# Kernel optimization log

Hardware: AMD Instinct MI355X
Metric: run time of the kernel (lower is better)

Reference implementation:

```python
import jax, jax.numpy as jnp
import numpy as np

TAU = 0.5  # routing_temperature


def setup_inputs() -> dict:
    key = jax.random.key(0)
    ks = jax.random.split(key, 12)
    B, N, D = 8, 4096, 384  # d_inner = 384, grid 64x64
    G = 4
    s = 0.02
    inp = {
        "x": jax.random.normal(ks[0], (B, N, D), dtype=jnp.float32),
        "W_stream1": jax.random.normal(ks[1], (D, D), dtype=jnp.float32) * s,
        "b_stream1": jnp.zeros((D,), dtype=jnp.float32),
        "W_stream2": jax.random.normal(ks[2], (D, G), dtype=jnp.float32) * s,
        "b_stream2": jnp.zeros((G,), dtype=jnp.float32),
        "self_bias": jnp.full((1, G, 1, 1), 2.0, dtype=jnp.float32),
        "W_ga": jax.random.normal(ks[3], (D, D), dtype=jnp.float32) * s,
        "b_ga": jnp.full((D,), 1.5, dtype=jnp.float32),
        "W_gb": jax.random.normal(ks[4], (D, D), dtype=jnp.float32) * s,
        "b_gb": jnp.full((D,), -1.5, dtype=jnp.float32),
        "W_inj": jax.random.normal(ks[5], (D, 2 * D), dtype=jnp.float32) * s,
        "W_state": jax.random.normal(ks[6], (D, 2 * D), dtype=jnp.float32) * s,
        "W_out": jax.random.normal(ks[7], (2 * D, D), dtype=jnp.float32) * s,
        "D_skip": jnp.ones((D,), dtype=jnp.float32),
        "k_steps": 4,
    }
    return inp


def reference(x, W_stream1, b_stream1, W_stream2, b_stream2, self_bias,
              W_ga, b_ga, W_gb, b_gb, W_inj, W_state, W_out, D_skip, k_steps):
    B, N, D = x.shape
    h = w = int(round(N ** 0.5))
    G = self_bias.shape[1]
    C = D // G

    def to_grid(t):  # (B, N, F) -> (B, F, h, w)
        return jnp.transpose(t, (0, 2, 1)).reshape(B, -1, h, w)

    # state (U, V)
    uv = x @ W_state
    u, v = jnp.split(uv, 2, axis=-1)
    u, v = to_grid(u), to_grid(v)

    # stream function -> divergence-free velocity (discrete curl)
    psi = to_grid(jax.nn.silu(x @ W_stream1 + b_stream1) @ W_stream2 + b_stream2)
    psi_h = jnp.pad(psi, ((0, 0), (0, 0), (1, 1), (0, 0)))
    vx = 0.5 * (psi_h[:, :, 2:, :] - psi_h[:, :, :-2, :])
    psi_w = jnp.pad(psi, ((0, 0), (0, 0), (0, 0), (1, 1)))
    vy = -0.5 * (psi_w[:, :, :, 2:] - psi_w[:, :, :, :-2])

    # 5-neighbor routing: [self, up, down, left, right]
    logits = jnp.stack([
        jnp.broadcast_to(self_bias, vx.shape),
        -vx / TAU, vx / TAU, -vy / TAU, vy / TAU,
    ], axis=2)  # (B, G, 5, h, w)
    routing = jax.nn.softmax(logits, axis=2)

    gate_a = to_grid(jax.nn.sigmoid(x @ W_ga + b_ga))
    gate_b = to_grid(jax.nn.sigmoid(x @ W_gb + b_gb))

    inj = x @ W_inj
    xu, xv = jnp.split(inj, 2, axis=-1)
    xu, xv = to_grid(xu), to_grid(xv)

    def transport(state):  # (B, D, h, w)
        sp_h = jnp.pad(state, ((0, 0), (0, 0), (1, 1), (0, 0)))
        s_up, s_down = sp_h[:, :, :-2, :], sp_h[:, :, 2:, :]
        sp_w = jnp.pad(state, ((0, 0), (0, 0), (0, 0), (1, 1)))
        s_left, s_right = sp_w[:, :, :, :-2], sp_w[:, :, :, 2:]
        nb = jnp.stack([state, s_up, s_down, s_left, s_right], axis=2)  # (B,D,5,h,w)
        nb = nb.reshape(B, G, C, 5, h, w)
        out = jnp.einsum('bgcnhw,bgnhw->bgchw', nb, routing)
        return out.reshape(B, D, h, w)

    for _ in range(int(k_steps)):
        u = gate_a * transport(u) + gate_b * xu
        v = gate_a * transport(v) + gate_b * xv

    u_out = jnp.transpose(u.reshape(B, D, N), (0, 2, 1))
    v_out = jnp.transpose(v.reshape(B, D, N), (0, 2, 1))
    combined = jnp.concatenate([u_out, v_out], axis=-1)
    return combined @ W_out + x * D_skip
```

## Files before the change

### kernel.cpp

```cpp
#include <hip/hip_runtime.h>
#include <hip/hip_bf16.h>

typedef __attribute__((ext_vector_type(8))) short bf16x8;
typedef __attribute__((ext_vector_type(4))) short short4v;
typedef __attribute__((ext_vector_type(4))) float f32x4;

#define TAU_INV 2.0f

__device__ __forceinline__ short f2bf(float f) {
  unsigned u = __float_as_uint(f);
  u += 0x7fffu + ((u >> 16) & 1u);
  return (short)(u >> 16);
}
__device__ __forceinline__ float bf2f(short s) {
  return __uint_as_float(((unsigned)(unsigned short)s) << 16);
}

__global__ __launch_bounds__(256) void prep_weights(
    const float* __restrict__ w_state, const float* __restrict__ w_inj,
    const float* __restrict__ w_ga, const float* __restrict__ w_gb,
    const float* __restrict__ w_s1, const float* __restrict__ w_out,
    short* __restrict__ t_state, short* __restrict__ t_inj,
    short* __restrict__ t_ga, short* __restrict__ t_gb,
    short* __restrict__ t_s1, short* __restrict__ t_out)
{
  int idx = blockIdx.x * 256 + threadIdx.x;
  const float* src; short* dst; int C, K;
  if (idx < 294912)                  { src = w_state; dst = t_state; C = 768; K = 384; }
  else if ((idx -= 294912) < 294912) { src = w_inj;   dst = t_inj;   C = 768; K = 384; }
  else if ((idx -= 294912) < 147456) { src = w_ga;    dst = t_ga;    C = 384; K = 384; }
  else if ((idx -= 147456) < 147456) { src = w_gb;    dst = t_gb;    C = 384; K = 384; }
  else if ((idx -= 147456) < 147456) { src = w_s1;    dst = t_s1;    C = 384; K = 384; }
  else           { idx -= 147456;      src = w_out;   dst = t_out;   C = 384; K = 768; }
  int c = idx / K, k = idx - c * K;
  dst[c * K + k] = f2bf(src[k * C + c]);
}

template<int EP>
__global__ __launch_bounds__(256) void gemm_x(
    const float* __restrict__ X, const short* __restrict__ Wt,
    const float* __restrict__ bias,
    short* __restrict__ out0, short* __restrict__ out1)
{
  __shared__ short As[128 * 72];
  __shared__ short Bs[128 * 72];
  const int tid = threadIdx.x;
  const int lane = tid & 63;
  const int wv = tid >> 6;
  const int wr = wv >> 1, wc = wv & 1;
  const int m0 = blockIdx.x * 128, c0 = blockIdx.y * 128;
  const int l15 = lane & 15, l4 = lane >> 4;
  f32x4 acc[4][4] = {};
  for (int k0 = 0; k0 < 384; k0 += 64) {
    __syncthreads();
#pragma unroll
    for (int i = 0; i < 8; ++i) {
      int q = tid + i * 256;
      int m = q >> 4, kq = (q & 15) * 4;
      const float4 xv = *(const float4*)(X + (m0 + m) * 384 + k0 + kq);
      short4v s;
      s[0] = f2bf(xv.x); s[1] = f2bf(xv.y); s[2] = f2bf(xv.z); s[3] = f2bf(xv.w);
      *(short4v*)(As + m * 72 + kq) = s;
    }
#pragma unroll
    for (int i = 0; i < 4; ++i) {
      int h = tid + i * 256;
      int c = h >> 3, kc = (h & 7) * 8;
      bf16x8 wvv = *(const bf16x8*)(Wt + (c0 + c) * 384 + k0 + kc);
      *(bf16x8*)(Bs + c * 72 + kc) = wvv;
    }
    __syncthreads();
#pragma unroll
    for (int kk = 0; kk < 2; ++kk) {
      bf16x8 af[4], bfv[4];
#pragma unroll
      for (int f = 0; f < 4; ++f) {
        af[f]  = *(const bf16x8*)(As + (wr * 64 + f * 16 + l15) * 72 + kk * 32 + l4 * 8);
        bfv[f] = *(const bf16x8*)(Bs + (wc * 64 + f * 16 + l15) * 72 + kk * 32 + l4 * 8);
      }
#pragma unroll
      for (int i = 0; i < 4; ++i)
#pragma unroll
        for (int j = 0; j < 4; ++j)
          acc[i][j] = __builtin_amdgcn_mfma_f32_16x16x32_bf16(af[i], bfv[j], acc[i][j], 0, 0, 0);
    }
  }
#pragma unroll
  for (int i = 0; i < 4; ++i) {
#pragma unroll
    for (int j = 0; j < 4; ++j) {
      const int c = c0 + wc * 64 + j * 16 + l15;
      const int mb = m0 + wr * 64 + i * 16 + l4 * 4;
      f32x4 v = acc[i][j];
      if (EP == 0) {
        short4v s;
        s[0] = f2bf(v[0]); s[1] = f2bf(v[1]); s[2] = f2bf(v[2]); s[3] = f2bf(v[3]);
        int b = mb >> 12, n = mb & 4095;
        short* base = (c < 384) ? out0 : out1;
        int plane = (c >= 384) ? (c - 384) : c;
        *(short4v*)(base + (b * 384 + plane) * 4096 + n) = s;
      } else if (EP == 1) {
        float bb = bias[c];
        short4v s;
#pragma unroll
        for (int r = 0; r < 4; ++r) {
          float t = v[r] + bb;
          t = 1.f / (1.f + __expf(-t));
          s[r] = f2bf(t);
        }
        int b = mb >> 12, n = mb & 4095;
        *(short4v*)(out0 + (b * 384 + c) * 4096 + n) = s;
      } else {
        float bb = bias[c];
#pragma unroll
        for (int r = 0; r < 4; ++r) {
          float t = v[r] + bb;
          float sg = 1.f / (1.f + __expf(-t));
          out0[(mb + r) * 384 + c] = f2bf(t * sg);
        }
      }
    }
  }
}

__global__ __launch_bounds__(256) void psi_kernel(
    const short* __restrict__ S1, const float* __restrict__ W2,
    const float* __restrict__ b2, float* __restrict__ psi)
{
  const int lane = threadIdx.x & 63;
  const int wv = threadIdx.x >> 6;
  const int m = blockIdx.x * 4 + wv;
  float a0 = 0.f, a1 = 0.f, a2 = 0.f, a3 = 0.f;
#pragma unroll
  for (int t = 0; t < 6; ++t) {
    int k = lane + t * 64;
    float sv = bf2f(S1[m * 384 + k]);
    float4 wr = *(const float4*)(W2 + k * 4);
    a0 += sv * wr.x; a1 += sv * wr.y; a2 += sv * wr.z; a3 += sv * wr.w;
  }
  for (int off = 32; off > 0; off >>= 1) {
    a0 += __shfl_down(a0, off, 64);
    a1 += __shfl_down(a1, off, 64);
    a2 += __shfl_down(a2, off, 64);
    a3 += __shfl_down(a3, off, 64);
  }
  if (lane == 0) {
    int bb = m >> 12, n = m & 4095;
    psi[(bb * 4 + 0) * 4096 + n] = a0 + b2[0];
    psi[(bb * 4 + 1) * 4096 + n] = a1 + b2[1];
    psi[(bb * 4 + 2) * 4096 + n] = a2 + b2[2];
    psi[(bb * 4 + 3) * 4096 + n] = a3 + b2[3];
  }
}

__global__ __launch_bounds__(256) void routing_kernel(
    const float* __restrict__ psi, const float* __restrict__ sb,
    float* __restrict__ R)
{
  const int idx = blockIdx.x * 256 + threadIdx.x;
  const int n = idx & 4095, bg = idx >> 12;
  const int i = n >> 6, j = n & 63;
  const float* p = psi + bg * 4096;
  float up = (i > 0)  ? p[n - 64] : 0.f;
  float dn = (i < 63) ? p[n + 64] : 0.f;
  float lf = (j > 0)  ? p[n - 1]  : 0.f;
  float rt = (j < 63) ? p[n + 1]  : 0.f;
  float vx = 0.5f * (dn - up);
  float vy = -0.5f * (rt - lf);
  float l0 = sb[bg & 3];
  float l1 = -vx * TAU_INV, l2 = vx * TAU_INV, l3 = -vy * TAU_INV, l4v = vy * TAU_INV;
  float mx = fmaxf(fmaxf(fmaxf(l0, l1), fmaxf(l2, l3)), l4v);
  float e0 = __expf(l0 - mx), e1 = __expf(l1 - mx), e2 = __expf(l2 - mx);
  float e3 = __expf(l3 - mx), e4 = __expf(l4v - mx);
  float inv = 1.f / (e0 + e1 + e2 + e3 + e4);
  const int NP = 8 * 4 * 4096;
  R[0 * NP + idx] = e0 * inv;
  R[1 * NP + idx] = e1 * inv;
  R[2 * NP + idx] = e2 * inv;
  R[3 * NP + idx] = e3 * inv;
  R[4 * NP + idx] = e4 * inv;
}

__global__ __launch_bounds__(512, 2) void transport_kernel(
    short* __restrict__ Ug, short* __restrict__ Vg,
    const short* __restrict__ Ga, const short* __restrict__ Gb,
    const short* __restrict__ Xu, const short* __restrict__ Xv,
    const float* __restrict__ R, const int* __restrict__ ksp)
{
  __shared__ float su[4096];
  __shared__ float sv[4096];
  const int tid = threadIdx.x;
  const int bd = blockIdx.x;
  const int b = bd / 384;
  const int d = bd - b * 384;
  const int g = d / 96;
  const int pbase = bd * 4096;
  const int rbase = (b * 4 + g) * 4096;
  const int NP = 8 * 4 * 4096;
  const int p0 = tid * 8;
  const int i = tid >> 3;
  const int j0 = (tid & 7) * 8;
  const int s = i & 7;

  float ga[8], gb[8], xu[8], xv[8], r0[8], r1[8], r2[8], r3[8], r4[8];
  {
    bf16x8 t;
    t = *(const bf16x8*)(Ga + pbase + p0);
#pragma unroll
    for (int c = 0; c < 8; ++c) ga[c] = bf2f(t[c]);
    t = *(const bf16x8*)(Gb + pbase + p0);
#pragma unroll
    for (int c = 0; c < 8; ++c) gb[c] = bf2f(t[c]);
    t = *(const bf16x8*)(Xu + pbase + p0);
#pragma unroll
    for (int c = 0; c < 8; ++c) xu[c] = bf2f(t[c]);
    t = *(const bf16x8*)(Xv + pbase + p0);
#pragma unroll
    for (int c = 0; c < 8; ++c) xv[c] = bf2f(t[c]);
  }
#pragma unroll
  for (int q = 0; q < 2; ++q) {
    float4 f0 = *(const float4*)(R + 0 * NP + rbase + p0 + q * 4);
    float4 f1 = *(const float4*)(R + 1 * NP + rbase + p0 + q * 4);
    float4 f2 = *(const float4*)(R + 2 * NP + rbase + p0 + q * 4);
    float4 f3 = *(const float4*)(R + 3 * NP + rbase + p0 + q * 4);
    float4 f4 = *(const float4*)(R + 4 * NP + rbase + p0 + q * 4);
    r0[q*4+0]=f0.x; r0[q*4+1]=f0.y; r0[q*4+2]=f0.z; r0[q*4+3]=f0.w;
    r1[q*4+0]=f1.x; r1[q*4+1]=f1.y; r1[q*4+2]=f1.z; r1[q*4+3]=f1.w;
    r2[q*4+0]=f2.x; r2[q*4+1]=f2.y; r2[q*4+2]=f2.z; r2[q*4+3]=f2.w;
    r3[q*4+0]=f3.x; r3[q*4+1]=f3.y; r3[q*4+2]=f3.z; r3[q*4+3]=f3.w;
    r4[q*4+0]=f4.x; r4[q*4+1]=f4.y; r4[q*4+2]=f4.z; r4[q*4+3]=f4.w;
  }
  {
    bf16x8 tu = *(const bf16x8*)(Ug + pbase + p0);
    bf16x8 tv = *(const bf16x8*)(Vg + pbase + p0);
#pragma unroll
    for (int c = 0; c < 8; ++c) { su[p0 + (c ^ s)] = bf2f(tu[c]); sv[p0 + (c ^ s)] = bf2f(tv[c]); }
  }
  __syncthreads();
  const int ks = ksp[0];
  const bool hasUp = (i > 0), hasDn = (i < 63);
  const int sU = (i - 1) & 7, sD = (i + 1) & 7;
  for (int step = 0; step < ks; ++step) {
    float cu[8], cv[8], nu[8], nv[8];
#pragma unroll
    for (int c = 0; c < 8; ++c) { cu[c] = su[p0 + (c ^ s)]; cv[c] = sv[p0 + (c ^ s)]; }
    float luu = (j0 > 0)  ? su[(p0 - 1) ^ s] : 0.f;
    float luv = (j0 > 0)  ? sv[(p0 - 1) ^ s] : 0.f;
    float ruu = (j0 < 56) ? su[(p0 + 8) ^ s] : 0.f;
    float ruv = (j0 < 56) ? sv[(p0 + 8) ^ s] : 0.f;
#pragma unroll
    for (int c = 0; c < 8; ++c) {
      float upU = hasUp ? su[(p0 - 64) + (c ^ sU)] : 0.f;
      float upV = hasUp ? sv[(p0 - 64) + (c ^ sU)] : 0.f;
      float dnU = hasDn ? su[(p0 + 64) + (c ^ sD)] : 0.f;
      float dnV = hasDn ? sv[(p0 + 64) + (c ^ sD)] : 0.f;
      float lfU = (c > 0) ? cu[c - 1] : luu;
      float lfV = (c > 0) ? cv[c - 1] : luv;
      float rtU = (c < 7) ? cu[c + 1] : ruu;
      float rtV = (c < 7) ? cv[c + 1] : ruv;
      nu[c] = ga[c] * (r0[c]*cu[c] + r1[c]*upU + r2[c]*dnU + r3[c]*lfU + r4[c]*rtU) + gb[c]*xu[c];
      nv[c] = ga[c] * (r0[c]*cv[c] + r1[c]*upV + r2[c]*dnV + r3[c]*lfV + r4[c]*rtV) + gb[c]*xv[c];
    }
    __syncthreads();
#pragma unroll
    for (int c = 0; c < 8; ++c) { su[p0 + (c ^ s)] = nu[c]; sv[p0 + (c ^ s)] = nv[c]; }
    __syncthreads();
  }
  bf16x8 ou, ov;
#pragma unroll
  for (int c = 0; c < 8; ++c) { ou[c] = f2bf(su[p0 + (c ^ s)]); ov[c] = f2bf(sv[p0 + (c ^ s)]); }
  *(bf16x8*)(Ug + pbase + p0) = ou;
  *(bf16x8*)(Vg + pbase + p0) = ov;
}

__global__ __launch_bounds__(256) void gemm_final(
    const short* __restrict__ U, const short* __restrict__ V,
    const short* __restrict__ Wt, const float* __restrict__ X,
    const float* __restrict__ Dskip, float* __restrict__ out)
{
  __shared__ short As[64 * 128];
  __shared__ short Bs[128 * 72];
  const int tid = threadIdx.x;
  const int lane = tid & 63;
  const int wv = tid >> 6, wr = wv >> 1, wc = wv & 1;
  const int m0 = blockIdx.x * 128, c0 = blockIdx.y * 128;
  const int b = m0 >> 12, n0 = m0 & 4095;
  const int l15 = lane & 15, l4 = lane >> 4;
  f32x4 acc[4][4] = {};
  for (int k0 = 0; k0 < 768; k0 += 64) {
    const short* src = (k0 < 384) ? U : V;
    const int kp = (k0 >= 384) ? (k0 - 384) : k0;
    __syncthreads();
#pragma unroll
    for (int i = 0; i < 4; ++i) {
      int h = tid + i * 256;
      int k = h >> 4, cc = h & 15;
      bf16x8 tv = *(const bf16x8*)(src + (b * 384 + kp + k) * 4096 + n0 + cc * 8);
      int ccs = cc ^ (((k >> 3) & 3) << 1);
      *(bf16x8*)(As + k * 128 + ccs * 8) = tv;
    }
#pragma unroll
    for (int i = 0; i < 4; ++i) {
      int h = tid + i * 256;
      int c = h >> 3, kc = (h & 7) * 8;
      bf16x8 wvv = *(const bf16x8*)(Wt + (c0 + c) * 768 + k0 + kc);
      *(bf16x8*)(Bs + c * 72 + kc) = wvv;
    }
    __syncthreads();
#pragma unroll
    for (int kk = 0; kk < 2; ++kk) {
      bf16x8 af[4], bfv[4];
#pragma unroll
      for (int f = 0; f < 4; ++f) {
        const int mm = wr * 64 + f * 16 + l15;
        const int chunk = mm >> 3, wi = mm & 7;
        bf16x8 av;
#pragma unroll
        for (int jj = 0; jj < 8; ++jj) {
          int k = kk * 32 + l4 * 8 + jj;
          int ccs = chunk ^ (((k >> 3) & 3) << 1);
          av[jj] = As[k * 128 + ccs * 8 + wi];
        }
        af[f] = av;
        bfv[f] = *(const bf16x8*)(Bs + (wc * 64 + f * 16 + l15) * 72 + kk * 32 + l4 * 8);
      }
#pragma unroll
      for (int i = 0; i < 4; ++i)
#pragma unroll
        for (int j = 0; j < 4; ++j)
          acc[i][j] = __builtin_amdgcn_mfma_f32_16x16x32_bf16(af[i], bfv[j], acc[i][j], 0, 0, 0);
    }
  }
#pragma unroll
  for (int i = 0; i < 4; ++i)
#pragma unroll
    for (int j = 0; j < 4; ++j) {
      const int c = c0 + wc * 64 + j * 16 + l15;
      const int mb = m0 + wr * 64 + i * 16 + l4 * 4;
      const float ds = Dskip[c];
#pragma unroll
      for (int r = 0; r < 4; ++r) {
        int idx = (mb + r) * 384 + c;
        out[idx] = acc[i][j][r] + X[idx] * ds;
      }
    }
}

extern "C" void kernel_launch(void* const* d_in, const int* in_sizes, int n_in,
                              void* d_out, int out_size, void* d_ws, size_t ws_size,
                              hipStream_t stream) {
  (void)in_sizes; (void)n_in; (void)out_size; (void)ws_size;
  const float* x       = (const float*)d_in[0];
  const float* w_s1    = (const float*)d_in[1];
  const float* b_s1    = (const float*)d_in[2];
  const float* w_s2    = (const float*)d_in[3];
  const float* b_s2    = (const float*)d_in[4];
  const float* sb      = (const float*)d_in[5];
  const float* w_ga    = (const float*)d_in[6];
  const float* b_ga    = (const float*)d_in[7];
  const float* w_gb    = (const float*)d_in[8];
  const float* b_gb    = (const float*)d_in[9];
  const float* w_inj   = (const float*)d_in[10];
  const float* w_state = (const float*)d_in[11];
  const float* w_out   = (const float*)d_in[12];
  const float* dskip   = (const float*)d_in[13];
  const int*   ksp     = (const int*)d_in[14];
  float* out = (float*)d_out;

  char* ws = (char*)d_ws;
  size_t off = 0;
  auto alloc = [&](size_t bytes) -> void* {
    void* p = ws + off;
    off += (bytes + 255) & ~(size_t)255;
    return p;
  };
  short* t_state = (short*)alloc(768 * 384 * 2);
  short* t_inj   = (short*)alloc(768 * 384 * 2);
  short* t_ga    = (short*)alloc(384 * 384 * 2);
  short* t_gb    = (short*)alloc(384 * 384 * 2);
  short* t_s1    = (short*)alloc(384 * 384 * 2);
  short* t_out   = (short*)alloc(384 * 768 * 2);
  const size_t PL = (size_t)8 * 384 * 4096;
  short* ug  = (short*)alloc(PL * 2);
  short* vg  = (short*)alloc(PL * 2);
  short* xug = (short*)alloc(PL * 2);
  short* xvg = (short*)alloc(PL * 2);
  short* gag = (short*)alloc(PL * 2);
  short* gbg = (short*)alloc(PL * 2);
  short* s1  = (short*)alloc(PL * 2);
  float* psi = (float*)alloc((size_t)8 * 4 * 4096 * 4);
  float* R   = (float*)alloc((size_t)5 * 8 * 4 * 4096 * 4);

  prep_weights<<<dim3(5184), dim3(256), 0, stream>>>(
      w_state, w_inj, w_ga, w_gb, w_s1, w_out,
      t_state, t_inj, t_ga, t_gb, t_s1, t_out);
  gemm_x<0><<<dim3(256, 6), dim3(256), 0, stream>>>(x, t_state, nullptr, ug, vg);
  gemm_x<0><<<dim3(256, 6), dim3(256), 0, stream>>>(x, t_inj, nullptr, xug, xvg);
  gemm_x<1><<<dim3(256, 3), dim3(256), 0, stream>>>(x, t_ga, b_ga, gag, nullptr);
  gemm_x<1><<<dim3(256, 3), dim3(256), 0, stream>>>(x, t_gb, b_gb, gbg, nullptr);
  gemm_x<2><<<dim3(256, 3), dim3(256), 0, stream>>>(x, t_s1, b_s1, s1, nullptr);
  psi_kernel<<<dim3(8192), dim3(256), 0, stream>>>(s1, w_s2, b_s2, psi);
  routing_kernel<<<dim3(512), dim3(256), 0, stream>>>(psi, sb, R);
  transport_kernel<<<dim3(3072), dim3(512), 0, stream>>>(ug, vg, gag, gbg, xug, xvg, R, ksp);
  gemm_final<<<dim3(256, 3), dim3(256), 0, stream>>>(ug, vg, t_out, x, dskip, out);
}
```

Measured before the change: 462.5 us.

## Fuse input GEMMs into one launch, pre-convert x to bf16, double-buffer transport LDS

The five input projections now share one concatenated bf16 weight matrix and run as a single GEMM launch. A separate kernel converts x to bf16 once, so each GEMM tile no longer re-converts fp32 x. The transport kernel folds the gate_a and gate_b factors into precomputed coefficients and keeps the current state in registers. It interleaves u and v as float2 in a double-buffered LDS array, which drops one barrier per step, and raises its occupancy hint. In exchange it uses an extra bf16 copy of x and adds branchier epilogue routing, and the higher occupancy bound may constrain registers.

New measurement: 709.7 us. 1.53x slower.

```diff
diff --git a/kernel.cpp b/kernel.cpp
--- a/kernel.cpp
+++ b/kernel.cpp
@@ -20,27 +20,47 @@
     const float* __restrict__ w_state, const float* __restrict__ w_inj,
     const float* __restrict__ w_ga, const float* __restrict__ w_gb,
     const float* __restrict__ w_s1, const float* __restrict__ w_out,
-    short* __restrict__ t_state, short* __restrict__ t_inj,
-    short* __restrict__ t_ga, short* __restrict__ t_gb,
-    short* __restrict__ t_s1, short* __restrict__ t_out)
+    short* __restrict__ t_cat, short* __restrict__ t_out)
 {
   int idx = blockIdx.x * 256 + threadIdx.x;
-  const float* src; short* dst; int C, K;
-  if (idx < 294912)                  { src = w_state; dst = t_state; C = 768; K = 384; }
-  else if ((idx -= 294912) < 294912) { src = w_inj;   dst = t_inj;   C = 768; K = 384; }
-  else if ((idx -= 294912) < 147456) { src = w_ga;    dst = t_ga;    C = 384; K = 384; }
-  else if ((idx -= 147456) < 147456) { src = w_gb;    dst = t_gb;    C = 384; K = 384; }
-  else if ((idx -= 147456) < 147456) { src = w_s1;    dst = t_s1;    C = 384; K = 384; }
-  else           { idx -= 147456;      src = w_out;   dst = t_out;   C = 384; K = 768; }
-  int c = idx / K, k = idx - c * K;
-  dst[c * K + k] = f2bf(src[k * C + c]);
-}
-
-template<int EP>
-__global__ __launch_bounds__(256) void gemm_x(
-    const float* __restrict__ X, const short* __restrict__ Wt,
-    const float* __restrict__ bias,
-    short* __restrict__ out0, short* __restrict__ out1)
+  const int NCAT = 2688 * 384;
+  if (idx < NCAT) {
+    int c = idx / 384, k = idx - c * 384;
+    float v;
+    if (c < 768)        v = w_state[k * 768 + c];
+    else if (c < 1536)  v = w_inj[k * 768 + (c - 768)];
+    else if (c < 1920)  v = w_ga[k * 384 + (c - 1536)];
+    else if (c < 2304)  v = w_gb[k * 384 + (c - 1920)];
+    else                v = w_s1[k * 384 + (c - 2304)];
+    t_cat[idx] = f2bf(v);
+  } else {
+    int j = idx - NCAT;
+    int c = j / 768, k = j - c * 768;
+    t_out[c * 768 + k] = f2bf(w_out[k * 384 + c]);
+  }
+}
+
+__global__ __launch_bounds__(256) void prep_x(
+    const float* __restrict__ X, short* __restrict__ Xb)
+{
+  int t = blockIdx.x * 256 + threadIdx.x;
+  int base = t * 8;
+  float4 a = *(const float4*)(X + base);
+  float4 b = *(const float4*)(X + base + 4);
+  bf16x8 s;
+  s[0] = f2bf(a.x); s[1] = f2bf(a.y); s[2] = f2bf(a.z); s[3] = f2bf(a.w);
+  s[4] = f2bf(b.x); s[5] = f2bf(b.y); s[6] = f2bf(b.z); s[7] = f2bf(b.w);
+  *(bf16x8*)(Xb + base) = s;
+}
+
+__global__ __launch_bounds__(256) void gemm_fused(
+    const short* __restrict__ Xb, const short* __restrict__ Wt,
+    const float* __restrict__ b_ga, const float* __restrict__ b_gb,
+    const float* __restrict__ b_s1,
+    short* __restrict__ ug, short* __restrict__ vg,
+    short* __restrict__ xug, short* __restrict__ xvg,
+    short* __restrict__ gag, short* __restrict__ gbg,
+    short* __restrict__ s1)
 {
   __shared__ short As[128 * 72];
   __shared__ short Bs[128 * 72];
@@ -54,13 +74,11 @@
   for (int k0 = 0; k0 < 384; k0 += 64) {
     __syncthreads();
 #pragma unroll
-    for (int i = 0; i < 8; ++i) {
-      int q = tid + i * 256;
-      int m = q >> 4, kq = (q & 15) * 4;
-      const float4 xv = *(const float4*)(X + (m0 + m) * 384 + k0 + kq);
-      short4v s;
-      s[0] = f2bf(xv.x); s[1] = f2bf(xv.y); s[2] = f2bf(xv.z); s[3] = f2bf(xv.w);
-      *(short4v*)(As + m * 72 + kq) = s;
+    for (int i = 0; i < 4; ++i) {
+      int h = tid + i * 256;
+      int m = h >> 3, kc = (h & 7) * 8;
+      bf16x8 xv = *(const bf16x8*)(Xb + (m0 + m) * 384 + k0 + kc);
+      *(bf16x8*)(As + m * 72 + kc) = xv;
     }
 #pragma unroll
     for (int i = 0; i < 4; ++i) {
@@ -91,32 +109,37 @@
     for (int j = 0; j < 4; ++j) {
       const int c = c0 + wc * 64 + j * 16 + l15;
       const int mb = m0 + wr * 64 + i * 16 + l4 * 4;
+      const int b = mb >> 12, n = mb & 4095;
       f32x4 v = acc[i][j];
-      if (EP == 0) {
+      if (c < 1536) {
+        int cc = (c >= 768) ? (c - 768) : c;
+        short* base;
+        if (c < 768) base = (cc < 384) ? ug : vg;
+        else         base = (cc < 384) ? xug : xvg;
+        int plane = (cc >= 384) ? (cc - 384) : cc;
         short4v s;
         s[0] = f2bf(v[0]); s[1] = f2bf(v[1]); s[2] = f2bf(v[2]); s[3] = f2bf(v[3]);
-        int b = mb >> 12, n = mb & 4095;
-        short* base = (c < 384) ? out0 : out1;
-        int plane = (c >= 384) ? (c - 384) : c;
         *(short4v*)(base + (b * 384 + plane) * 4096 + n) = s;
-      } else if (EP == 1) {
-        float bb = bias[c];
+      } else if (c < 2304) {
+        const float* bias = (c < 1920) ? b_ga : b_gb;
+        short* base = (c < 1920) ? gag : gbg;
+        int plane = (c < 1920) ? (c - 1536) : (c - 1920);
+        float bb = bias[plane];
         short4v s;
 #pragma unroll
         for (int r = 0; r < 4; ++r) {
           float t = v[r] + bb;
-          t = 1.f / (1.f + __expf(-t));
-          s[r] = f2bf(t);
+          s[r] = f2bf(1.f / (1.f + __expf(-t)));
         }
-        int b = mb >> 12, n = mb & 4095;
-        *(short4v*)(out0 + (b * 384 + c) * 4096 + n) = s;
+        *(short4v*)(base + (b * 384 + plane) * 4096 + n) = s;
       } else {
-        float bb = bias[c];
+        int plane = c - 2304;
+        float bb = b_s1[plane];
 #pragma unroll
         for (int r = 0; r < 4; ++r) {
           float t = v[r] + bb;
           float sg = 1.f / (1.f + __expf(-t));
-          out0[(mb + r) * 384 + c] = f2bf(t * sg);
+          s1[(mb + r) * 384 + plane] = f2bf(t * sg);
         }
       }
     }
@@ -181,14 +204,13 @@
   R[4 * NP + idx] = e4 * inv;
 }
 
-__global__ __launch_bounds__(512, 2) void transport_kernel(
+__global__ __launch_bounds__(512, 4) void transport_kernel(
     short* __restrict__ Ug, short* __restrict__ Vg,
     const short* __restrict__ Ga, const short* __restrict__ Gb,
     const short* __restrict__ Xu, const short* __restrict__ Xv,
     const float* __restrict__ R, const int* __restrict__ ksp)
 {
-  __shared__ float su[4096];
-  __shared__ float sv[4096];
+  __shared__ float2 sb[2][4096];
   const int tid = threadIdx.x;
   const int bd = blockIdx.x;
   const int b = bd / 384;
@@ -202,8 +224,10 @@
   const int j0 = (tid & 7) * 8;
   const int s = i & 7;
 
-  float ga[8], gb[8], xu[8], xv[8], r0[8], r1[8], r2[8], r3[8], r4[8];
+  float ar0[8], ar1[8], ar2[8], ar3[8], ar4[8], bxu[8], bxv[8];
+  float cu[8], cv[8];
   {
+    float ga[8], gb[8];
     bf16x8 t;
     t = *(const bf16x8*)(Ga + pbase + p0);
 #pragma unroll
@@ -213,63 +237,64 @@
     for (int c = 0; c < 8; ++c) gb[c] = bf2f(t[c]);
     t = *(const bf16x8*)(Xu + pbase + p0);
 #pragma unroll
-    for (int c = 0; c < 8; ++c) xu[c] = bf2f(t[c]);
+    for (int c = 0; c < 8; ++c) bxu[c] = gb[c] * bf2f(t[c]);
     t = *(const bf16x8*)(Xv + pbase + p0);
 #pragma unroll
-    for (int c = 0; c < 8; ++c) xv[c] = bf2f(t[c]);
-  }
-#pragma unroll
-  for (int q = 0; q < 2; ++q) {
-    float4 f0 = *(const float4*)(R + 0 * NP + rbase + p0 + q * 4);
-    float4 f1 = *(const float4*)(R + 1 * NP + rbase + p0 + q * 4);
-    float4 f2 = *(const float4*)(R + 2 * NP + rbase + p0 + q * 4);
-    float4 f3 = *(const float4*)(R + 3 * NP + rbase + p0 + q * 4);
-    float4 f4 = *(const float4*)(R + 4 * NP + rbase + p0 + q * 4);
-    r0[q*4+0]=f0.x; r0[q*4+1]=f0.y; r0[q*4+2]=f0.z; r0[q*4+3]=f0.w;
-    r1[q*4+0]=f1.x; r1[q*4+1]=f1.y; r1[q*4+2]=f1.z; r1[q*4+3]=f1.w;
-    r2[q*4+0]=f2.x; r2[q*4+1]=f2.y; r2[q*4+2]=f2.z; r2[q*4+3]=f2.w;
-    r3[q*4+0]=f3.x; r3[q*4+1]=f3.y; r3[q*4+2]=f3.z; r3[q*4+3]=f3.w;
-    r4[q*4+0]=f4.x; r4[q*4+1]=f4.y; r4[q*4+2]=f4.z; r4[q*4+3]=f4.w;
-  }
-  {
+    for (int c = 0; c < 8; ++c) bxv[c] = gb[c] * bf2f(t[c]);
+#pragma unroll
+    for (int q = 0; q < 2; ++q) {
+      float4 f0 = *(const float4*)(R + 0 * NP + rbase + p0 + q * 4);
+      float4 f1 = *(const float4*)(R + 1 * NP + rbase + p0 + q * 4);
+      float4 f2 = *(const float4*)(R + 2 * NP + rbase + p0 + q * 4);
+      float4 f3 = *(const float4*)(R + 3 * NP + rbase + p0 + q * 4);
+      float4 f4 = *(const float4*)(R + 4 * NP + rbase + p0 + q * 4);
+      ar0[q*4+0]=ga[q*4+0]*f0.x; ar0[q*4+1]=ga[q*4+1]*f0.y; ar0[q*4+2]=ga[q*4+2]*f0.z; ar0[q*4+3]=ga[q*4+3]*f0.w;
+      ar1[q*4+0]=ga[q*4+0]*f1.x; ar1[q*4+1]=ga[q*4+1]*f1.y; ar1[q*4+2]=ga[q*4+2]*f1.z; ar1[q*4+3]=ga[q*4+3]*f1.w;
+      ar2[q*4+0]=ga[q*4+0]*f2.x; ar2[q*4+1]=ga[q*4+1]*f2.y; ar2[q*4+2]=ga[q*4+2]*f2.z; ar2[q*4+3]=ga[q*4+3]*f2.w;
+      ar3[q*4+0]=ga[q*4+0]*f3.x; ar3[q*4+1]=ga[q*4+1]*f3.y; ar3[q*4+2]=ga[q*4+2]*f3.z; ar3[q*4+3]=ga[q*4+3]*f3.w;
+      ar4[q*4+0]=ga[q*4+0]*f4.x; ar4[q*4+1]=ga[q*4+1]*f4.y; ar4[q*4+2]=ga[q*4+2]*f4.z; ar4[q*4+3]=ga[q*4+3]*f4.w;
+    }
     bf16x8 tu = *(const bf16x8*)(Ug + pbase + p0);
     bf16x8 tv = *(const bf16x8*)(Vg + pbase + p0);
 #pragma unroll
-    for (int c = 0; c < 8; ++c) { su[p0 + (c ^ s)] = bf2f(tu[c]); sv[p0 + (c ^ s)] = bf2f(tv[c]); }
+    for (int c = 0; c < 8; ++c) {
+      cu[c] = bf2f(tu[c]); cv[c] = bf2f(tv[c]);
+      sb[0][p0 + (c ^ s)] = make_float2(cu[c], cv[c]);
+    }
   }
   __syncthreads();
   const int ks = ksp[0];
   const bool hasUp = (i > 0), hasDn = (i < 63);
   const int sU = (i - 1) & 7, sD = (i + 1) & 7;
+  int cur = 0;
   for (int step = 0; step < ks; ++step) {
-    float cu[8], cv[8], nu[8], nv[8];
-#pragma unroll
-    for (int c = 0; c < 8; ++c) { cu[c] = su[p0 + (c ^ s)]; cv[c] = sv[p0 + (c ^ s)]; }
-    float luu = (j0 > 0)  ? su[(p0 - 1) ^ s] : 0.f;
-    float luv = (j0 > 0)  ? sv[(p0 - 1) ^ s] : 0.f;
-    float ruu = (j0 < 56) ? su[(p0 + 8) ^ s] : 0.f;
-    float ruv = (j0 < 56) ? sv[(p0 + 8) ^ s] : 0.f;
+    const float2* __restrict__ buf = sb[cur];
+    float2* __restrict__ nxt = sb[cur ^ 1];
+    float2 lfe = (j0 > 0)  ? buf[(p0 - 1) ^ s] : make_float2(0.f, 0.f);
+    float2 rte = (j0 < 56) ? buf[(p0 + 8) ^ s] : make_float2(0.f, 0.f);
+    float nu[8], nv[8];
 #pragma unroll
     for (int c = 0; c < 8; ++c) {
-      float upU = hasUp ? su[(p0 - 64) + (c ^ sU)] : 0.f;
-      float upV = hasUp ? sv[(p0 - 64) + (c ^ sU)] : 0.f;
-      float dnU = hasDn ? su[(p0 + 64) + (c ^ sD)] : 0.f;
-      float dnV = hasDn ? sv[(p0 + 64) + (c ^ sD)] : 0.f;
-      float lfU = (c > 0) ? cu[c - 1] : luu;
-      float lfV = (c > 0) ? cv[c - 1] : luv;
-      float rtU = (c < 7) ? cu[c + 1] : ruu;
-      float rtV = (c < 7) ? cv[c + 1] : ruv;
-      nu[c] = ga[c] * (r0[c]*cu[c] + r1[c]*upU + r2[c]*dnU + r3[c]*lfU + r4[c]*rtU) + gb[c]*xu[c];
-      nv[c] = ga[c] * (r0[c]*cv[c] + r1[c]*upV + r2[c]*dnV + r3[c]*lfV + r4[c]*rtV) + gb[c]*xv[c];
+      float2 up = hasUp ? buf[(p0 - 64) + (c ^ sU)] : make_float2(0.f, 0.f);
+      float2 dn = hasDn ? buf[(p0 + 64) + (c ^ sD)] : make_float2(0.f, 0.f);
+      float lfU = (c > 0) ? cu[c - 1] : lfe.x;
+      float lfV = (c > 0) ? cv[c - 1] : lfe.y;
+      float rtU = (c < 7) ? cu[c + 1] : rte.x;
+      float rtV = (c < 7) ? cv[c + 1] : rte.y;
+      nu[c] = ar0[c]*cu[c] + ar1[c]*up.x + ar2[c]*dn.x + ar3[c]*lfU + ar4[c]*rtU + bxu[c];
+      nv[c] = ar0[c]*cv[c] + ar1[c]*up.y + ar2[c]*dn.y + ar3[c]*lfV + ar4[c]*rtV + bxv[c];
+    }
+#pragma unroll
+    for (int c = 0; c < 8; ++c) {
+      nxt[p0 + (c ^ s)] = make_float2(nu[c], nv[c]);
+      cu[c] = nu[c]; cv[c] = nv[c];
     }
     __syncthreads();
-#pragma unroll
-    for (int c = 0; c < 8; ++c) { su[p0 + (c ^ s)] = nu[c]; sv[p0 + (c ^ s)] = nv[c]; }
-    __syncthreads();
+    cur ^= 1;
   }
   bf16x8 ou, ov;
 #pragma unroll
-  for (int c = 0; c < 8; ++c) { ou[c] = f2bf(su[p0 + (c ^ s)]); ov[c] = f2bf(sv[p0 + (c ^ s)]); }
+  for (int c = 0; c < 8; ++c) { ou[c] = f2bf(cu[c]); ov[c] = f2bf(cv[c]); }
   *(bf16x8*)(Ug + pbase + p0) = ou;
   *(bf16x8*)(Vg + pbase + p0) = ov;
 }
@@ -375,13 +400,10 @@
     off += (bytes + 255) & ~(size_t)255;
     return p;
   };
-  short* t_state = (short*)alloc(768 * 384 * 2);
-  short* t_inj   = (short*)alloc(768 * 384 * 2);
-  short* t_ga    = (short*)alloc(384 * 384 * 2);
-  short* t_gb    = (short*)alloc(384 * 384 * 2);
-  short* t_s1    = (short*)alloc(384 * 384 * 2);
-  short* t_out   = (short*)alloc(384 * 768 * 2);
+  short* t_cat = (short*)alloc((size_t)2688 * 384 * 2);
+  short* t_out = (short*)alloc((size_t)384 * 768 * 2);
   const size_t PL = (size_t)8 * 384 * 4096;
+  short* xb  = (short*)alloc(PL * 2);
   short* ug  = (short*)alloc(PL * 2);
   short* vg  = (short*)alloc(PL * 2);
   short* xug = (short*)alloc(PL * 2);
@@ -393,13 +415,10 @@
   float* R   = (float*)alloc((size_t)5 * 8 * 4 * 4096 * 4);
 
   prep_weights<<<dim3(5184), dim3(256), 0, stream>>>(
-      w_state, w_inj, w_ga, w_gb, w_s1, w_out,
-      t_state, t_inj, t_ga, t_gb, t_s1, t_out);
-  gemm_x<0><<<dim3(256, 6), dim3(256), 0, stream>>>(x, t_state, nullptr, ug, vg);
-  gemm_x<0><<<dim3(256, 6), dim3(256), 0, stream>>>(x, t_inj, nullptr, xug, xvg);
-  gemm_x<1><<<dim3(256, 3), dim3(256), 0, stream>>>(x, t_ga, b_ga, gag, nullptr);
-  gemm_x<1><<<dim3(256, 3), dim3(256), 0, stream>>>(x, t_gb, b_gb, gbg, nullptr);
-  gemm_x<2><<<dim3(256, 3), dim3(256), 0, stream>>>(x, t_s1, b_s1, s1, nullptr);
+      w_state, w_inj, w_ga, w_gb, w_s1, w_out, t_cat, t_out);
+  prep_x<<<dim3(6144), dim3(256), 0, stream>>>(x, xb);
+  gemm_fused<<<dim3(256, 21), dim3(256), 0, stream>>>(
+      xb, t_cat, b_ga, b_gb, b_s1, ug, vg, xug, xvg, gag, gbg, s1);
   psi_kernel<<<dim3(8192), dim3(256), 0, stream>>>(s1, w_s2, b_s2, psi);
   routing_kernel<<<dim3(512), dim3(256), 0, stream>>>(psi, sb, R);
   transport_kernel<<<dim3(3072), dim3(512), 0, stream>>>(ug, vg, gag, gbg, xug, xvg, R, ksp);
```
